# Kernel tuning notes

Hardware: AMD Instinct MI355X
Metric: run time of the kernel (lower is better)

The kernel has to match this reference:

```python
import jax, jax.numpy as jnp
import numpy as np

V, E, H, M = 32000, 512, 1024, 256
B, S = 2, 1024


def setup_inputs() -> dict:
    key = jax.random.key(0)
    ks = jax.random.split(key, 12)
    def rn(k, shape, scale=0.02):
        return jax.random.normal(k, shape, jnp.float32) * scale
    return dict(
        input_ids=jax.random.randint(ks[0], (B, S), 0, V),
        emb_W=rn(ks[1], (V, E)),
        w_ih=rn(ks[2], (3 * H, E)), w_hh=rn(ks[3], (3 * H, H)),
        b_ih=jnp.zeros((3 * H,), jnp.float32), b_hh=jnp.zeros((3 * H,), jnp.float32),
        Wq=rn(ks[4], (M, H)), bq=jnp.zeros((M,), jnp.float32),
        Wk=rn(ks[5], (M, H)), bk=jnp.zeros((M,), jnp.float32),
        Wg=rn(ks[6], (1, H)), bg=jnp.zeros((1,), jnp.float32),
        W1=rn(ks[7], (4 * E, H)), b1=jnp.zeros((4 * E,), jnp.float32),
        W2=rn(ks[8], (E, 4 * E)), b2=jnp.zeros((E,), jnp.float32),
        Wr=rn(ks[9], (E, E)), br=jnp.zeros((E,), jnp.float32),
        memory_scale=jnp.array(6.0, jnp.float32),
        output_bias=jnp.zeros((V,), jnp.float32),
    )


def _gru(emb, w_ih, w_hh, b_ih, b_hh):
    # PyTorch GRU gate order: r, z, n
    Bb = emb.shape[0]
    Hh = w_hh.shape[1]
    xp = emb @ w_ih.T + b_ih  # [B,S,3H], input projections precomputed
    def step(h, xt):
        gh = h @ w_hh.T + b_hh
        ir, iz, inn = jnp.split(xt, 3, axis=-1)
        hr, hz, hn = jnp.split(gh, 3, axis=-1)
        r = jax.nn.sigmoid(ir + hr)
        z = jax.nn.sigmoid(iz + hz)
        n = jnp.tanh(inn + r * hn)
        h = (1.0 - z) * n + z * h
        return h, h
    h0 = jnp.zeros((Bb, Hh), emb.dtype)
    _, hs = jax.lax.scan(step, h0, jnp.swapaxes(xp, 0, 1))
    return jnp.swapaxes(hs, 0, 1)  # [B,S,H]


def reference(input_ids, emb_W, w_ih, w_hh, b_ih, b_hh, Wq, bq, Wk, bk, Wg, bg,
              W1, b1, W2, b2, Wr, br, memory_scale, output_bias):
    Bb, Ss = input_ids.shape
    emb = emb_W[input_ids]                                   # [B,S,E]
    states = _gru(emb, w_ih, w_hh, b_ih, b_hh)               # [B,S,H] (dropout=0 -> identity)
    hf = jnp.square(jax.nn.relu(states @ W1.T + b1))         # [B,S,4E]
    base = hf @ W2.T + b2                                    # [B,S,E]
    residual = jax.nn.relu(base @ Wr.T + br)                 # [B,S,E]
    base_logits = base @ emb_W.T + output_bias               # [B,S,V]
    residual_logits = residual @ emb_W.T                     # [B,S,V]
    gate = jax.nn.sigmoid(states @ Wg.T + bg)                # [B,S,1]
    q = states @ Wq.T + bq                                   # [B,S,M]
    k = states @ Wk.T + bk                                   # [B,S,M]
    scores = jnp.einsum('bqd,bkd->bqk', q, k) / jnp.sqrt(jnp.float32(q.shape[-1]))
    mask = jnp.tril(jnp.ones((Ss, Ss), bool), k=-1)          # strictly-causal (diag excluded)
    scores = jnp.where(mask, scores, jnp.finfo(scores.dtype).min)
    attn = jax.nn.softmax(scores, axis=-1) * mask
    attn = attn / jnp.maximum(attn.sum(axis=-1, keepdims=True), 1e-6)
    gated = attn * (gate * memory_scale)                     # [B,S,S]
    bi = jnp.arange(Bb)[:, None, None]
    si = jnp.arange(Ss)[None, :, None]
    vi = jnp.broadcast_to(input_ids[:, None, :], (Bb, Ss, Ss))
    base_logits = base_logits.at[bi, si, vi].add(gated)      # scatter_add into vocab by token id
    return base_logits + gate * residual_logits
```

## Files before the change

### kernel.cpp

```cpp
#include <hip/hip_runtime.h>
#include <math.h>

typedef __attribute__((ext_vector_type(8))) short bf16x8;
typedef __attribute__((ext_vector_type(4))) float f32x4;

__device__ __forceinline__ unsigned short f2bf(float x) {
    unsigned u = __float_as_uint(x);
    unsigned r = (u + 0x7FFF + ((u >> 16) & 1)) >> 16;
    return (unsigned short)r;
}
__device__ __forceinline__ float bf_lo(unsigned u) { return __uint_as_float(u << 16); }
__device__ __forceinline__ float bf_hi(unsigned u) { return __uint_as_float(u & 0xffff0000u); }

#define ACT_NONE  0
#define ACT_RELU  1
#define ACT_RELU2 2

template <int ACT, bool GATHER, bool TRANSOUT>
__global__ __launch_bounds__(256) void gemm_bt(
    const float* __restrict__ A, const float* __restrict__ Bm,
    const float* __restrict__ bias, float* __restrict__ C,
    const int* __restrict__ ids, int M, int N, int K)
{
    __shared__ unsigned short as_[64][40];
    __shared__ unsigned short bs_[64][40];

    const int tid = threadIdx.x;
    const int bm = blockIdx.x, bn = blockIdx.y;
    const int r = tid >> 2, seg = tid & 3;

    const int arow = bm * 64 + r;
    const float* aptr = GATHER ? (A + (size_t)ids[arow] * K) : (A + (size_t)arow * K);
    const float* bptr = Bm + (size_t)(bn * 64 + r) * K;

    const int w = tid >> 6, lane = tid & 63;
    const int wr = w >> 1, wc = w & 1;
    const int al = lane & 15, kq = lane >> 4;

    f32x4 acc[2][2];
    for (int mi = 0; mi < 2; ++mi)
        for (int ni = 0; ni < 2; ++ni)
            acc[mi][ni] = (f32x4){0.f, 0.f, 0.f, 0.f};

    for (int k0 = 0; k0 < K; k0 += 32) {
        __syncthreads();
        {
            const float4* ap4 = (const float4*)(aptr + k0 + seg * 8);
            float4 a0 = ap4[0], a1 = ap4[1];
            uint4 pk;
            pk.x = (unsigned)f2bf(a0.x) | ((unsigned)f2bf(a0.y) << 16);
            pk.y = (unsigned)f2bf(a0.z) | ((unsigned)f2bf(a0.w) << 16);
            pk.z = (unsigned)f2bf(a1.x) | ((unsigned)f2bf(a1.y) << 16);
            pk.w = (unsigned)f2bf(a1.z) | ((unsigned)f2bf(a1.w) << 16);
            *(uint4*)&as_[r][seg * 8] = pk;

            const float4* bp4 = (const float4*)(bptr + k0 + seg * 8);
            float4 b0 = bp4[0], b1 = bp4[1];
            pk.x = (unsigned)f2bf(b0.x) | ((unsigned)f2bf(b0.y) << 16);
            pk.y = (unsigned)f2bf(b0.z) | ((unsigned)f2bf(b0.w) << 16);
            pk.z = (unsigned)f2bf(b1.x) | ((unsigned)f2bf(b1.y) << 16);
            pk.w = (unsigned)f2bf(b1.z) | ((unsigned)f2bf(b1.w) << 16);
            *(uint4*)&bs_[r][seg * 8] = pk;
        }
        __syncthreads();

        bf16x8 af[2], bfr[2];
        af[0]  = *(const bf16x8*)&as_[wr * 32 + al][kq * 8];
        af[1]  = *(const bf16x8*)&as_[wr * 32 + 16 + al][kq * 8];
        bfr[0] = *(const bf16x8*)&bs_[wc * 32 + al][kq * 8];
        bfr[1] = *(const bf16x8*)&bs_[wc * 32 + 16 + al][kq * 8];

        for (int mi = 0; mi < 2; ++mi)
            for (int ni = 0; ni < 2; ++ni)
                acc[mi][ni] = __builtin_amdgcn_mfma_f32_16x16x32_bf16(
                    af[mi], bfr[ni], acc[mi][ni], 0, 0, 0);
    }

    for (int mi = 0; mi < 2; ++mi) {
        for (int ni = 0; ni < 2; ++ni) {
            const int gcol = bn * 64 + wc * 32 + ni * 16 + al;
            const float bv = bias ? bias[gcol] : 0.f;
            for (int i = 0; i < 4; ++i) {
                const int grow = bm * 64 + wr * 32 + mi * 16 + kq * 4 + i;
                float v = acc[mi][ni][i] + bv;
                if (ACT == ACT_RELU)  v = fmaxf(v, 0.f);
                if (ACT == ACT_RELU2) { v = fmaxf(v, 0.f); v = v * v; }
                if (TRANSOUT) {
                    const int b = grow >> 10, s = grow & 1023;
                    C[((size_t)b * N + gcol) * 1024 + s] = v;
                } else {
                    C[(size_t)grow * N + gcol] = v;
                }
            }
        }
    }
}

__global__ void init_ws(float* hbuf, int* flags) {
    int t = blockIdx.x * 256 + threadIdx.x;
    if (t < 4096) hbuf[t] = 0.f;
    if (t < 128 * 32) flags[t] = 0;
}

__global__ __launch_bounds__(256, 1) void gru_kernel(
    const float* __restrict__ xp,
    const float* __restrict__ w_hh,
    const float* __restrict__ b_hh,
    float* __restrict__ states,
    float* __restrict__ hbuf,
    int* __restrict__ flags)
{
    __shared__ unsigned short wlds[24 * 1024];
    __shared__ float ghs[24][2];
    __shared__ float bh[24];

    const int wg = blockIdx.x, tid = threadIdx.x;
    const int u0 = wg * 8;

    for (int idx = tid; idx < 24 * 1024; idx += 256) {
        const int rr = idx >> 10, kk = idx & 1023;
        const int grow = (rr < 8) ? (u0 + rr) : (rr < 16) ? (1024 + u0 + rr - 8) : (2048 + u0 + rr - 16);
        wlds[idx] = f2bf(w_hh[((size_t)grow << 10) | kk]);
    }
    if (tid < 24) {
        const int rr = tid;
        const int grow = (rr < 8) ? (u0 + rr) : (rr < 16) ? (1024 + u0 + rr - 8) : (2048 + u0 + rr - 16);
        bh[rr] = b_hh[grow];
    }
    __syncthreads();

    const int w = tid >> 6, lane = tid & 63;
    const int j = tid & 7, bb = (tid >> 3) & 1;
    const float* xbase = xp + ((size_t)(bb << 10)) * 3072 + u0 + j;
    float hprev = 0.f;

    for (int t = 0; t < 1024; ++t) {
        const int p = t & 1;
        const float* src = hbuf + p * 2048;
        float* dst = hbuf + (1 - p) * 2048;

        float ir = 0.f, iz = 0.f, inn = 0.f;
        if (tid < 16) {
            const float* xr = xbase + (size_t)t * 3072;
            ir = xr[0]; iz = xr[1024]; inn = xr[2048];
        }

        if (w == 0 && t > 0) {
            const int need = t;
            for (;;) {
                int f0 = __hip_atomic_load(&flags[lane << 5],
                                           __ATOMIC_RELAXED, __HIP_MEMORY_SCOPE_AGENT);
                int f1 = __hip_atomic_load(&flags[(64 + lane) << 5],
                                           __ATOMIC_RELAXED, __HIP_MEMORY_SCOPE_AGENT);
                if (__all(f0 >= need && f1 >= need)) break;
            }
        }
        __syncthreads();

        f32x4 h_[8];
        {
            const char* pa = (const char*)src + ((size_t)lane << 5);
            const char* pb = pa + 4096;
            asm volatile(
                "global_load_dwordx4 %0, %8, off sc0 sc1\n\t"
                "global_load_dwordx4 %1, %8, off offset:16 sc0 sc1\n\t"
                "global_load_dwordx4 %2, %8, off offset:2048 sc0 sc1\n\t"
                "global_load_dwordx4 %3, %8, off offset:2064 sc0 sc1\n\t"
                "global_load_dwordx4 %4, %9, off sc0 sc1\n\t"
                "global_load_dwordx4 %5, %9, off offset:16 sc0 sc1\n\t"
                "global_load_dwordx4 %6, %9, off offset:2048 sc0 sc1\n\t"
                "global_load_dwordx4 %7, %9, off offset:2064 sc0 sc1\n\t"
                "s_waitcnt vmcnt(0)"
                : "=&v"(h_[0]), "=&v"(h_[1]), "=&v"(h_[2]), "=&v"(h_[3]),
                  "=&v"(h_[4]), "=&v"(h_[5]), "=&v"(h_[6]), "=&v"(h_[7])
                : "v"(pa), "v"(pb)
                : "memory");
        }

        float pacc[6][2];
        #pragma unroll
        for (int rr6 = 0; rr6 < 6; ++rr6) {
            pacc[rr6][0] = 0.f; pacc[rr6][1] = 0.f;
            const uint4* wr4 = (const uint4*)&wlds[(w * 6 + rr6) << 10];
            #pragma unroll
            for (int c = 0; c < 2; ++c) {
                const uint4 wv = wr4[c * 64 + lane];
                const float w0 = bf_lo(wv.x), w1 = bf_hi(wv.x);
                const float w2 = bf_lo(wv.y), w3 = bf_hi(wv.y);
                const float w4 = bf_lo(wv.z), w5 = bf_hi(wv.z);
                const float w6 = bf_lo(wv.w), w7 = bf_hi(wv.w);
                {
                    const f32x4 ha = h_[c * 2], hb2 = h_[c * 2 + 1];
                    pacc[rr6][0] += w0 * ha.x + w1 * ha.y + w2 * ha.z + w3 * ha.w
                                  + w4 * hb2.x + w5 * hb2.y + w6 * hb2.z + w7 * hb2.w;
                }
                {
                    const f32x4 ha = h_[4 + c * 2], hb2 = h_[4 + c * 2 + 1];
                    pacc[rr6][1] += w0 * ha.x + w1 * ha.y + w2 * ha.z + w3 * ha.w
                                  + w4 * hb2.x + w5 * hb2.y + w6 * hb2.z + w7 * hb2.w;
                }
            }
        }
        #pragma unroll
        for (int off = 32; off > 0; off >>= 1) {
            #pragma unroll
            for (int rr6 = 0; rr6 < 6; ++rr6) {
                pacc[rr6][0] += __shfl_xor(pacc[rr6][0], off);
                pacc[rr6][1] += __shfl_xor(pacc[rr6][1], off);
            }
        }
        if (lane == 0) {
            #pragma unroll
            for (int rr6 = 0; rr6 < 6; ++rr6) {
                ghs[w * 6 + rr6][0] = pacc[rr6][0];
                ghs[w * 6 + rr6][1] = pacc[rr6][1];
            }
        }
        __syncthreads();

        if (tid < 16) {
            const float hr  = ghs[j][bb]      + bh[j];
            const float hz  = ghs[8 + j][bb]  + bh[8 + j];
            const float hnv = ghs[16 + j][bb] + bh[16 + j];
            const float rg = 1.f / (1.f + __expf(-(ir + hr)));
            const float zg = 1.f / (1.f + __expf(-(iz + hz)));
            const float ng = tanhf(inn + rg * hnv);
            const float hnew = (1.f - zg) * ng + zg * hprev;
            hprev = hnew;
            const int row = (bb << 10) | t;
            states[(size_t)row * 1024 + u0 + j] = hnew;
            __hip_atomic_store(&dst[(bb << 10) + u0 + j], hnew,
                               __ATOMIC_RELAXED, __HIP_MEMORY_SCOPE_AGENT);
        }
        if (w == 0) {
            asm volatile("s_waitcnt vmcnt(0)" ::: "memory");
            if (lane == 0)
                __hip_atomic_store(&flags[wg << 5], t + 1,
                                   __ATOMIC_RELAXED, __HIP_MEMORY_SCOPE_AGENT);
        }
    }
}

__global__ __launch_bounds__(256) void gate_kernel(
    const float* __restrict__ states, const float* __restrict__ Wg,
    const float* __restrict__ bg, float* __restrict__ gate)
{
    const int w = threadIdx.x >> 6, lane = threadIdx.x & 63;
    const int row = blockIdx.x * 4 + w;
    const float4* sr = (const float4*)(states + (size_t)row * 1024);
    const float4* wr = (const float4*)Wg;
    float p = 0.f;
    for (int c = 0; c < 4; ++c) {
        const float4 sv = sr[c * 64 + lane];
        const float4 wv = wr[c * 64 + lane];
        p += sv.x * wv.x + sv.y * wv.y + sv.z * wv.z + sv.w * wv.w;
    }
    for (int off = 32; off > 0; off >>= 1) p += __shfl_xor(p, off);
    if (lane == 0) gate[row] = 1.f / (1.f + __expf(-(p + bg[0])));
}

__global__ __launch_bounds__(256) void combined_kernel(
    const float* __restrict__ base, const float* __restrict__ resid,
    const float* __restrict__ gate, float* __restrict__ comb)
{
    const int idx = blockIdx.x * 256 + threadIdx.x;
    const int row = idx >> 9;
    comb[idx] = base[idx] + gate[row] * resid[idx];
}

__global__ __launch_bounds__(256) void attn_scatter(
    const float* __restrict__ q,
    const float* __restrict__ kT,
    const float* __restrict__ gate,
    const float* __restrict__ mscale,
    const int* __restrict__ ids,
    float* __restrict__ out)
{
    const int i = blockIdx.x, b = blockIdx.y, t = threadIdx.x;
    if (i == 0) return;
    __shared__ float qs[256];
    __shared__ float red[256];

    qs[t] = q[((size_t)((b << 10) | i)) * 256 + t];
    __syncthreads();

    const int j0 = t * 4;
    float s[4] = {0.f, 0.f, 0.f, 0.f};
    const float* kb = kT + (size_t)b * 256 * 1024;
    if (j0 < i) {
        for (int kk = 0; kk < 256; ++kk) {
            const float qv = qs[kk];
            const float4 kv = *(const float4*)(kb + (size_t)kk * 1024 + j0);
            s[0] += qv * kv.x; s[1] += qv * kv.y; s[2] += qv * kv.z; s[3] += qv * kv.w;
        }
    }
    const float scale = 0.0625f;
    float mx = -1e30f;
    for (int e = 0; e < 4; ++e)
        if (j0 + e < i) { s[e] *= scale; mx = fmaxf(mx, s[e]); }

    red[t] = mx; __syncthreads();
    for (int o = 128; o > 0; o >>= 1) {
        if (t < o) red[t] = fmaxf(red[t], red[t + o]);
        __syncthreads();
    }
    const float m = red[0];
    __syncthreads();

    float p[4]; float ssum = 0.f;
    for (int e = 0; e < 4; ++e) {
        if (j0 + e < i) { p[e] = __expf(s[e] - m); ssum += p[e]; }
        else p[e] = 0.f;
    }
    red[t] = ssum; __syncthreads();
    for (int o = 128; o > 0; o >>= 1) {
        if (t < o) red[t] += red[t + o];
        __syncthreads();
    }
    const float denom = fmaxf(red[0], 1e-6f);
    const float g6 = gate[(b << 10) | i] * mscale[0] / denom;

    float* orow = out + ((size_t)((b << 10) | i)) * 32000;
    const int* idr = ids + (b << 10);
    for (int e = 0; e < 4; ++e)
        if (j0 + e < i) atomicAdd(&orow[idr[j0 + e]], p[e] * g6);
}

extern "C" void kernel_launch(void* const* d_in, const int* in_sizes, int n_in,
                              void* d_out, int out_size, void* d_ws, size_t ws_size,
                              hipStream_t stream)
{
    const int*   ids     = (const int*)  d_in[0];
    const float* emb_W   = (const float*)d_in[1];
    const float* w_ih    = (const float*)d_in[2];
    const float* w_hh    = (const float*)d_in[3];
    const float* b_ih    = (const float*)d_in[4];
    const float* b_hh    = (const float*)d_in[5];
    const float* Wq      = (const float*)d_in[6];
    const float* bq      = (const float*)d_in[7];
    const float* Wk      = (const float*)d_in[8];
    const float* bk      = (const float*)d_in[9];
    const float* Wg      = (const float*)d_in[10];
    const float* bg      = (const float*)d_in[11];
    const float* W1      = (const float*)d_in[12];
    const float* b1      = (const float*)d_in[13];
    const float* W2      = (const float*)d_in[14];
    const float* b2      = (const float*)d_in[15];
    const float* Wr      = (const float*)d_in[16];
    const float* br      = (const float*)d_in[17];
    const float* mscale  = (const float*)d_in[18];
    const float* out_b   = (const float*)d_in[19];
    float* out = (float*)d_out;

    float* ws = (float*)d_ws;
    float* xp     = ws;
    float* states = xp     + (size_t)2048 * 3072;
    float* hf     = states + (size_t)2048 * 1024;
    float* base   = hf     + (size_t)2048 * 2048;
    float* resid  = base   + (size_t)2048 * 512;
    float* qv     = resid  + (size_t)2048 * 512;
    float* kT     = qv     + (size_t)2048 * 256;
    float* comb   = kT     + (size_t)2 * 256 * 1024;
    float* gate   = comb   + (size_t)2048 * 512;
    float* hbuf   = gate   + 2048;
    int*   flags  = (int*)(hbuf + 4096);

    dim3 blk(256);

    gemm_bt<ACT_NONE, true, false><<<dim3(32, 48), blk, 0, stream>>>(
        emb_W, w_ih, b_ih, xp, ids, 2048, 3072, 512);

    init_ws<<<16, blk, 0, stream>>>(hbuf, flags);
    gru_kernel<<<128, blk, 0, stream>>>(xp, w_hh, b_hh, states, hbuf, flags);

    gemm_bt<ACT_RELU2, false, false><<<dim3(32, 32), blk, 0, stream>>>(
        states, W1, b1, hf, nullptr, 2048, 2048, 1024);

    gemm_bt<ACT_NONE, false, false><<<dim3(32, 8), blk, 0, stream>>>(
        hf, W2, b2, base, nullptr, 2048, 512, 2048);

    gemm_bt<ACT_RELU, false, false><<<dim3(32, 8), blk, 0, stream>>>(
        base, Wr, br, resid, nullptr, 2048, 512, 512);

    gate_kernel<<<512, blk, 0, stream>>>(states, Wg, bg, gate);

    gemm_bt<ACT_NONE, false, false><<<dim3(32, 4), blk, 0, stream>>>(
        states, Wq, bq, qv, nullptr, 2048, 256, 1024);
    gemm_bt<ACT_NONE, false, true><<<dim3(32, 4), blk, 0, stream>>>(
        states, Wk, bk, kT, nullptr, 2048, 256, 1024);

    combined_kernel<<<4096, blk, 0, stream>>>(base, resid, gate, comb);

    gemm_bt<ACT_NONE, false, false><<<dim3(32, 500), blk, 0, stream>>>(
        comb, emb_W, out_b, out, nullptr, 2048, 32000, 512);

    attn_scatter<<<dim3(1024, 2), blk, 0, stream>>>(qv, kT, gate, mscale, ids, out);
}
```

Before: 4.237 ms.

## Fuse GRU step flags into hidden-state values as tagged pairs

Replaces the separate per-workgroup flag array and spin-then-load sequence in the persistent GRU kernel with (value, step tag) pairs written in one 8-byte store. Each wave now polls the hidden-state buffer directly until every tag matches the current step, which removes one global round trip and a block-wide barrier per timestep from the serial recurrence. It doubles the bytes read per poll, all four waves spin independently, and the ghs scratch is double-buffered because the barrier is gone.

```diff
diff --git a/kernel.cpp b/kernel.cpp
--- a/kernel.cpp
+++ b/kernel.cpp
@@ -96,10 +96,9 @@
     }
 }
 
-__global__ void init_ws(float* hbuf, int* flags) {
+__global__ void init_ws(float* hbuf2) {
     int t = blockIdx.x * 256 + threadIdx.x;
-    if (t < 4096) hbuf[t] = 0.f;
-    if (t < 128 * 32) flags[t] = 0;
+    if (t < 8192) hbuf2[t] = 0.f;
 }
 
 __global__ __launch_bounds__(256, 1) void gru_kernel(
@@ -107,11 +106,10 @@
     const float* __restrict__ w_hh,
     const float* __restrict__ b_hh,
     float* __restrict__ states,
-    float* __restrict__ hbuf,
-    int* __restrict__ flags)
+    float* __restrict__ hbuf2)
 {
     __shared__ unsigned short wlds[24 * 1024];
-    __shared__ float ghs[24][2];
+    __shared__ float ghs[2][24][2];
     __shared__ float bh[24];
 
     const int wg = blockIdx.x, tid = threadIdx.x;
@@ -136,8 +134,8 @@
 
     for (int t = 0; t < 1024; ++t) {
         const int p = t & 1;
-        const float* src = hbuf + p * 2048;
-        float* dst = hbuf + (1 - p) * 2048;
+        const float* src = hbuf2 + p * 4096;
+        float* dst = hbuf2 + (1 - p) * 4096;
 
         float ir = 0.f, iz = 0.f, inn = 0.f;
         if (tid < 16) {
@@ -145,36 +143,45 @@
             ir = xr[0]; iz = xr[1024]; inn = xr[2048];
         }
 
-        if (w == 0 && t > 0) {
-            const int need = t;
+        f32x4 q[16];
+        {
+            const char* b0 = (const char*)src + (lane << 6);
+            const char* b1 = b0 + 4096;
+            const char* b2 = b0 + 8192;
+            const char* b3 = b0 + 12288;
+            const int expect = t;
             for (;;) {
-                int f0 = __hip_atomic_load(&flags[lane << 5],
-                                           __ATOMIC_RELAXED, __HIP_MEMORY_SCOPE_AGENT);
-                int f1 = __hip_atomic_load(&flags[(64 + lane) << 5],
-                                           __ATOMIC_RELAXED, __HIP_MEMORY_SCOPE_AGENT);
-                if (__all(f0 >= need && f1 >= need)) break;
+                asm volatile(
+                    "global_load_dwordx4 %0, %16, off sc0 sc1\n\t"
+                    "global_load_dwordx4 %1, %16, off offset:16 sc0 sc1\n\t"
+                    "global_load_dwordx4 %2, %16, off offset:32 sc0 sc1\n\t"
+                    "global_load_dwordx4 %3, %16, off offset:48 sc0 sc1\n\t"
+                    "global_load_dwordx4 %4, %17, off sc0 sc1\n\t"
+                    "global_load_dwordx4 %5, %17, off offset:16 sc0 sc1\n\t"
+                    "global_load_dwordx4 %6, %17, off offset:32 sc0 sc1\n\t"
+                    "global_load_dwordx4 %7, %17, off offset:48 sc0 sc1\n\t"
+                    "global_load_dwordx4 %8, %18, off sc0 sc1\n\t"
+                    "global_load_dwordx4 %9, %18, off offset:16 sc0 sc1\n\t"
+                    "global_load_dwordx4 %10, %18, off offset:32 sc0 sc1\n\t"
+                    "global_load_dwordx4 %11, %18, off offset:48 sc0 sc1\n\t"
+                    "global_load_dwordx4 %12, %19, off sc0 sc1\n\t"
+                    "global_load_dwordx4 %13, %19, off offset:16 sc0 sc1\n\t"
+                    "global_load_dwordx4 %14, %19, off offset:32 sc0 sc1\n\t"
+                    "global_load_dwordx4 %15, %19, off offset:48 sc0 sc1\n\t"
+                    "s_waitcnt vmcnt(0)"
+                    : "=&v"(q[0]), "=&v"(q[1]), "=&v"(q[2]), "=&v"(q[3]),
+                      "=&v"(q[4]), "=&v"(q[5]), "=&v"(q[6]), "=&v"(q[7]),
+                      "=&v"(q[8]), "=&v"(q[9]), "=&v"(q[10]), "=&v"(q[11]),
+                      "=&v"(q[12]), "=&v"(q[13]), "=&v"(q[14]), "=&v"(q[15])
+                    : "v"(b0), "v"(b1), "v"(b2), "v"(b3)
+                    : "memory");
+                bool ok = true;
+                #pragma unroll
+                for (int k = 0; k < 16; ++k)
+                    ok = ok && (__float_as_int(q[k].y) == expect)
+                            && (__float_as_int(q[k].w) == expect);
+                if (__all(ok)) break;
             }
-        }
-        __syncthreads();
-
-        f32x4 h_[8];
-        {
-            const char* pa = (const char*)src + ((size_t)lane << 5);
-            const char* pb = pa + 4096;
-            asm volatile(
-                "global_load_dwordx4 %0, %8, off sc0 sc1\n\t"
-                "global_load_dwordx4 %1, %8, off offset:16 sc0 sc1\n\t"
-                "global_load_dwordx4 %2, %8, off offset:2048 sc0 sc1\n\t"
-                "global_load_dwordx4 %3, %8, off offset:2064 sc0 sc1\n\t"
-                "global_load_dwordx4 %4, %9, off sc0 sc1\n\t"
-                "global_load_dwordx4 %5, %9, off offset:16 sc0 sc1\n\t"
-                "global_load_dwordx4 %6, %9, off offset:2048 sc0 sc1\n\t"
-                "global_load_dwordx4 %7, %9, off offset:2064 sc0 sc1\n\t"
-                "s_waitcnt vmcnt(0)"
-                : "=&v"(h_[0]), "=&v"(h_[1]), "=&v"(h_[2]), "=&v"(h_[3]),
-                  "=&v"(h_[4]), "=&v"(h_[5]), "=&v"(h_[6]), "=&v"(h_[7])
-                : "v"(pa), "v"(pb)
-                : "memory");
         }
 
         float pacc[6][2];
@@ -189,16 +196,15 @@
                 const float w2 = bf_lo(wv.y), w3 = bf_hi(wv.y);
                 const float w4 = bf_lo(wv.z), w5 = bf_hi(wv.z);
                 const float w6 = bf_lo(wv.w), w7 = bf_hi(wv.w);
-                {
-                    const f32x4 ha = h_[c * 2], hb2 = h_[c * 2 + 1];
-                    pacc[rr6][0] += w0 * ha.x + w1 * ha.y + w2 * ha.z + w3 * ha.w
-                                  + w4 * hb2.x + w5 * hb2.y + w6 * hb2.z + w7 * hb2.w;
-                }
-                {
-                    const f32x4 ha = h_[4 + c * 2], hb2 = h_[4 + c * 2 + 1];
-                    pacc[rr6][1] += w0 * ha.x + w1 * ha.y + w2 * ha.z + w3 * ha.w
-                                  + w4 * hb2.x + w5 * hb2.y + w6 * hb2.z + w7 * hb2.w;
-                }
+                const int c4 = c * 4;
+                pacc[rr6][0] += w0 * q[c4].x     + w1 * q[c4].z
+                              + w2 * q[c4 + 1].x + w3 * q[c4 + 1].z
+                              + w4 * q[c4 + 2].x + w5 * q[c4 + 2].z
+                              + w6 * q[c4 + 3].x + w7 * q[c4 + 3].z;
+                pacc[rr6][1] += w0 * q[8 + c4].x     + w1 * q[8 + c4].z
+                              + w2 * q[8 + c4 + 1].x + w3 * q[8 + c4 + 1].z
+                              + w4 * q[8 + c4 + 2].x + w5 * q[8 + c4 + 2].z
+                              + w6 * q[8 + c4 + 3].x + w7 * q[8 + c4 + 3].z;
             }
         }
         #pragma unroll
@@ -212,16 +218,16 @@
         if (lane == 0) {
             #pragma unroll
             for (int rr6 = 0; rr6 < 6; ++rr6) {
-                ghs[w * 6 + rr6][0] = pacc[rr6][0];
-                ghs[w * 6 + rr6][1] = pacc[rr6][1];
+                ghs[p][w * 6 + rr6][0] = pacc[rr6][0];
+                ghs[p][w * 6 + rr6][1] = pacc[rr6][1];
             }
         }
         __syncthreads();
 
         if (tid < 16) {
-            const float hr  = ghs[j][bb]      + bh[j];
-            const float hz  = ghs[8 + j][bb]  + bh[8 + j];
-            const float hnv = ghs[16 + j][bb] + bh[16 + j];
+            const float hr  = ghs[p][j][bb]      + bh[j];
+            const float hz  = ghs[p][8 + j][bb]  + bh[8 + j];
+            const float hnv = ghs[p][16 + j][bb] + bh[16 + j];
             const float rg = 1.f / (1.f + __expf(-(ir + hr)));
             const float zg = 1.f / (1.f + __expf(-(iz + hz)));
             const float ng = tanhf(inn + rg * hnv);
@@ -229,14 +235,12 @@
             hprev = hnew;
             const int row = (bb << 10) | t;
             states[(size_t)row * 1024 + u0 + j] = hnew;
-            __hip_atomic_store(&dst[(bb << 10) + u0 + j], hnew,
-                               __ATOMIC_RELAXED, __HIP_MEMORY_SCOPE_AGENT);
-        }
-        if (w == 0) {
-            asm volatile("s_waitcnt vmcnt(0)" ::: "memory");
-            if (lane == 0)
-                __hip_atomic_store(&flags[wg << 5], t + 1,
-                                   __ATOMIC_RELAXED, __HIP_MEMORY_SCOPE_AGENT);
+            uint2 pk;
+            pk.x = __float_as_uint(hnew);
+            pk.y = (unsigned)(t + 1);
+            float* daddr = dst + 2 * ((bb << 10) + u0 + j);
+            asm volatile("global_store_dwordx2 %0, %1, off sc0 sc1"
+                         :: "v"(daddr), "v"(pk) : "memory");
         }
     }
 }
@@ -362,16 +366,15 @@
     float* kT     = qv     + (size_t)2048 * 256;
     float* comb   = kT     + (size_t)2 * 256 * 1024;
     float* gate   = comb   + (size_t)2048 * 512;
-    float* hbuf   = gate   + 2048;
-    int*   flags  = (int*)(hbuf + 4096);
+    float* hbuf2  = gate   + 2048;
 
     dim3 blk(256);
 
     gemm_bt<ACT_NONE, true, false><<<dim3(32, 48), blk, 0, stream>>>(
         emb_W, w_ih, b_ih, xp, ids, 2048, 3072, 512);
 
-    init_ws<<<16, blk, 0, stream>>>(hbuf, flags);
-    gru_kernel<<<128, blk, 0, stream>>>(xp, w_hh, b_hh, states, hbuf, flags);
+    init_ws<<<32, blk, 0, stream>>>(hbuf2);
+    gru_kernel<<<128, blk, 0, stream>>>(xp, w_hh, b_hh, states, hbuf2);
 
     gemm_bt<ACT_RELU2, false, false><<<dim3(32, 32), blk, 0, stream>>>(
         states, W1, b1, hf, nullptr, 2048, 2048, 1024);
```

Measured after the change: 7.662 ms. +80.8%, slower.

## Make each GRU wave compute its own units and drop per-step block barriers

Applied to the files above, without the earlier changes.

Each wave now owns two hidden units for both batch rows, with each half-wave handling one batch row. It computes the gate dot products, reduces them with shuffles within 32 lanes, and applies the GRU update locally. This removes both __syncthreads and the LDS staging of gate sums. Flags become packed per-wave counters (512 ints, read as two dwordx4 loads per lane), and every wave polls them itself. The weight layout in LDS is reshuffled to match the new lane mapping. The trade-offs are more polling traffic, since all four waves spin, and per-wave flag publishing.

```diff
diff --git a/kernel.cpp b/kernel.cpp
--- a/kernel.cpp
+++ b/kernel.cpp
@@ -3,6 +3,7 @@
 
 typedef __attribute__((ext_vector_type(8))) short bf16x8;
 typedef __attribute__((ext_vector_type(4))) float f32x4;
+typedef __attribute__((ext_vector_type(4))) int i32x4;
 
 __device__ __forceinline__ unsigned short f2bf(float x) {
     unsigned u = __float_as_uint(x);
@@ -99,7 +100,7 @@
 __global__ void init_ws(float* hbuf, int* flags) {
     int t = blockIdx.x * 256 + threadIdx.x;
     if (t < 4096) hbuf[t] = 0.f;
-    if (t < 128 * 32) flags[t] = 0;
+    if (t < 512) flags[t] = 0;
 }
 
 __global__ __launch_bounds__(256, 1) void gru_kernel(
@@ -111,132 +112,132 @@
     int* __restrict__ flags)
 {
     __shared__ unsigned short wlds[24 * 1024];
-    __shared__ float ghs[24][2];
-    __shared__ float bh[24];
 
     const int wg = blockIdx.x, tid = threadIdx.x;
     const int u0 = wg * 8;
+    const int w = tid >> 6, lane = tid & 63;
+    const int half = lane >> 5, hl = lane & 31;
 
     for (int idx = tid; idx < 24 * 1024; idx += 256) {
         const int rr = idx >> 10, kk = idx & 1023;
-        const int grow = (rr < 8) ? (u0 + rr) : (rr < 16) ? (1024 + u0 + rr - 8) : (2048 + u0 + rr - 16);
-        wlds[idx] = f2bf(w_hh[((size_t)grow << 10) | kk]);
-    }
-    if (tid < 24) {
-        const int rr = tid;
-        const int grow = (rr < 8) ? (u0 + rr) : (rr < 16) ? (1024 + u0 + rr - 8) : (2048 + u0 + rr - 16);
-        bh[rr] = b_hh[grow];
-    }
+        const int w_ = rr / 6, q = rr - 6 * w_;
+        const int g = q >> 1, u = q & 1;
+        const int grow = (g << 10) + u0 + 2 * w_ + u;
+        const int hl_ = kk >> 5, rem = kk & 31, c_ = rem >> 3, e = rem & 7;
+        wlds[(rr << 10) + c_ * 256 + hl_ * 8 + e] =
+            f2bf(w_hh[((size_t)grow << 10) | kk]);
+    }
+
+    const int uA = u0 + 2 * w;
+    const float2 bhr = *(const float2*)&b_hh[uA];
+    const float2 bhz = *(const float2*)&b_hh[1024 + uA];
+    const float2 bhn = *(const float2*)&b_hh[2048 + uA];
+
     __syncthreads();
 
-    const int w = tid >> 6, lane = tid & 63;
-    const int j = tid & 7, bb = (tid >> 3) & 1;
-    const float* xbase = xp + ((size_t)(bb << 10)) * 3072 + u0 + j;
-    float hprev = 0.f;
+    float hpA = 0.f, hpB = 0.f;
 
     for (int t = 0; t < 1024; ++t) {
         const int p = t & 1;
         const float* src = hbuf + p * 2048;
         float* dst = hbuf + (1 - p) * 2048;
 
-        float ir = 0.f, iz = 0.f, inn = 0.f;
-        if (tid < 16) {
-            const float* xr = xbase + (size_t)t * 3072;
-            ir = xr[0]; iz = xr[1024]; inn = xr[2048];
-        }
-
-        if (w == 0 && t > 0) {
+        float2 xr_ = make_float2(0.f, 0.f);
+        float2 xz_ = make_float2(0.f, 0.f);
+        float2 xn_ = make_float2(0.f, 0.f);
+        if (hl == 0) {
+            const float* xr = xp + (size_t)((half << 10) | t) * 3072 + uA;
+            xr_ = *(const float2*)xr;
+            xz_ = *(const float2*)(xr + 1024);
+            xn_ = *(const float2*)(xr + 2048);
+        }
+
+        if (t > 0) {
+            const char* fa = (const char*)flags + (lane << 5);
             const int need = t;
+            i32x4 f0, f1;
             for (;;) {
-                int f0 = __hip_atomic_load(&flags[lane << 5],
-                                           __ATOMIC_RELAXED, __HIP_MEMORY_SCOPE_AGENT);
-                int f1 = __hip_atomic_load(&flags[(64 + lane) << 5],
-                                           __ATOMIC_RELAXED, __HIP_MEMORY_SCOPE_AGENT);
-                if (__all(f0 >= need && f1 >= need)) break;
+                asm volatile(
+                    "global_load_dwordx4 %0, %2, off sc0 sc1\n\t"
+                    "global_load_dwordx4 %1, %2, off offset:16 sc0 sc1\n\t"
+                    "s_waitcnt vmcnt(0)"
+                    : "=&v"(f0), "=&v"(f1) : "v"(fa) : "memory");
+                int m = f0.x < f0.y ? f0.x : f0.y;
+                m = m < f0.z ? m : f0.z;  m = m < f0.w ? m : f0.w;
+                m = m < f1.x ? m : f1.x;  m = m < f1.y ? m : f1.y;
+                m = m < f1.z ? m : f1.z;  m = m < f1.w ? m : f1.w;
+                if (__all(m >= need)) break;
             }
         }
-        __syncthreads();
 
         f32x4 h_[8];
         {
-            const char* pa = (const char*)src + ((size_t)lane << 5);
-            const char* pb = pa + 4096;
+            const char* hb = (const char*)src + (half << 12) + (hl << 7);
             asm volatile(
                 "global_load_dwordx4 %0, %8, off sc0 sc1\n\t"
                 "global_load_dwordx4 %1, %8, off offset:16 sc0 sc1\n\t"
-                "global_load_dwordx4 %2, %8, off offset:2048 sc0 sc1\n\t"
-                "global_load_dwordx4 %3, %8, off offset:2064 sc0 sc1\n\t"
-                "global_load_dwordx4 %4, %9, off sc0 sc1\n\t"
-                "global_load_dwordx4 %5, %9, off offset:16 sc0 sc1\n\t"
-                "global_load_dwordx4 %6, %9, off offset:2048 sc0 sc1\n\t"
-                "global_load_dwordx4 %7, %9, off offset:2064 sc0 sc1\n\t"
+                "global_load_dwordx4 %2, %8, off offset:32 sc0 sc1\n\t"
+                "global_load_dwordx4 %3, %8, off offset:48 sc0 sc1\n\t"
+                "global_load_dwordx4 %4, %8, off offset:64 sc0 sc1\n\t"
+                "global_load_dwordx4 %5, %8, off offset:80 sc0 sc1\n\t"
+                "global_load_dwordx4 %6, %8, off offset:96 sc0 sc1\n\t"
+                "global_load_dwordx4 %7, %8, off offset:112 sc0 sc1\n\t"
                 "s_waitcnt vmcnt(0)"
                 : "=&v"(h_[0]), "=&v"(h_[1]), "=&v"(h_[2]), "=&v"(h_[3]),
                   "=&v"(h_[4]), "=&v"(h_[5]), "=&v"(h_[6]), "=&v"(h_[7])
-                : "v"(pa), "v"(pb)
+                : "v"(hb)
                 : "memory");
         }
 
-        float pacc[6][2];
+        float pacc[6];
         #pragma unroll
-        for (int rr6 = 0; rr6 < 6; ++rr6) {
-            pacc[rr6][0] = 0.f; pacc[rr6][1] = 0.f;
-            const uint4* wr4 = (const uint4*)&wlds[(w * 6 + rr6) << 10];
+        for (int q = 0; q < 6; ++q) {
+            const uint4* wr4 = (const uint4*)&wlds[(w * 6 + q) << 10];
+            float a = 0.f;
             #pragma unroll
-            for (int c = 0; c < 2; ++c) {
-                const uint4 wv = wr4[c * 64 + lane];
-                const float w0 = bf_lo(wv.x), w1 = bf_hi(wv.x);
-                const float w2 = bf_lo(wv.y), w3 = bf_hi(wv.y);
-                const float w4 = bf_lo(wv.z), w5 = bf_hi(wv.z);
-                const float w6 = bf_lo(wv.w), w7 = bf_hi(wv.w);
-                {
-                    const f32x4 ha = h_[c * 2], hb2 = h_[c * 2 + 1];
-                    pacc[rr6][0] += w0 * ha.x + w1 * ha.y + w2 * ha.z + w3 * ha.w
-                                  + w4 * hb2.x + w5 * hb2.y + w6 * hb2.z + w7 * hb2.w;
-                }
-                {
-                    const f32x4 ha = h_[4 + c * 2], hb2 = h_[4 + c * 2 + 1];
-                    pacc[rr6][1] += w0 * ha.x + w1 * ha.y + w2 * ha.z + w3 * ha.w
-                                  + w4 * hb2.x + w5 * hb2.y + w6 * hb2.z + w7 * hb2.w;
-                }
+            for (int c = 0; c < 4; ++c) {
+                const uint4 wv = wr4[c * 32 + hl];
+                const f32x4 ha = h_[c * 2], hb2 = h_[c * 2 + 1];
+                a += bf_lo(wv.x) * ha.x  + bf_hi(wv.x) * ha.y
+                   + bf_lo(wv.y) * ha.z  + bf_hi(wv.y) * ha.w
+                   + bf_lo(wv.z) * hb2.x + bf_hi(wv.z) * hb2.y
+                   + bf_lo(wv.w) * hb2.z + bf_hi(wv.w) * hb2.w;
             }
+            pacc[q] = a;
         }
         #pragma unroll
-        for (int off = 32; off > 0; off >>= 1) {
+        for (int off = 16; off > 0; off >>= 1) {
             #pragma unroll
-            for (int rr6 = 0; rr6 < 6; ++rr6) {
-                pacc[rr6][0] += __shfl_xor(pacc[rr6][0], off);
-                pacc[rr6][1] += __shfl_xor(pacc[rr6][1], off);
-            }
-        }
+            for (int q = 0; q < 6; ++q)
+                pacc[q] += __shfl_xor(pacc[q], off);
+        }
+
+        if (hl == 0) {
+            const float rA = 1.f / (1.f + __expf(-(xr_.x + pacc[0] + bhr.x)));
+            const float zA = 1.f / (1.f + __expf(-(xz_.x + pacc[2] + bhz.x)));
+            const float nA = tanhf(xn_.x + rA * (pacc[4] + bhn.x));
+            const float hA = (1.f - zA) * nA + zA * hpA;
+            hpA = hA;
+            const float rB = 1.f / (1.f + __expf(-(xr_.y + pacc[1] + bhr.y)));
+            const float zB = 1.f / (1.f + __expf(-(xz_.y + pacc[3] + bhz.y)));
+            const float nB = tanhf(xn_.y + rB * (pacc[5] + bhn.y));
+            const float hB = (1.f - zB) * nB + zB * hpB;
+            hpB = hB;
+
+            *(float2*)&states[(size_t)((half << 10) | t) * 1024 + uA] =
+                make_float2(hA, hB);
+
+            float2 hv = make_float2(hA, hB);
+            float* daddr = dst + (half << 10) + uA;
+            asm volatile("global_store_dwordx2 %0, %1, off sc0 sc1"
+                         :: "v"(daddr), "v"(hv) : "memory");
+        }
+        asm volatile("s_waitcnt vmcnt(0)" ::: "memory");
         if (lane == 0) {
-            #pragma unroll
-            for (int rr6 = 0; rr6 < 6; ++rr6) {
-                ghs[w * 6 + rr6][0] = pacc[rr6][0];
-                ghs[w * 6 + rr6][1] = pacc[rr6][1];
-            }
-        }
-        __syncthreads();
-
-        if (tid < 16) {
-            const float hr  = ghs[j][bb]      + bh[j];
-            const float hz  = ghs[8 + j][bb]  + bh[8 + j];
-            const float hnv = ghs[16 + j][bb] + bh[16 + j];
-            const float rg = 1.f / (1.f + __expf(-(ir + hr)));
-            const float zg = 1.f / (1.f + __expf(-(iz + hz)));
-            const float ng = tanhf(inn + rg * hnv);
-            const float hnew = (1.f - zg) * ng + zg * hprev;
-            hprev = hnew;
-            const int row = (bb << 10) | t;
-            states[(size_t)row * 1024 + u0 + j] = hnew;
-            __hip_atomic_store(&dst[(bb << 10) + u0 + j], hnew,
-                               __ATOMIC_RELAXED, __HIP_MEMORY_SCOPE_AGENT);
-        }
-        if (w == 0) {
-            asm volatile("s_waitcnt vmcnt(0)" ::: "memory");
-            if (lane == 0)
-                __hip_atomic_store(&flags[wg << 5], t + 1,
-                                   __ATOMIC_RELAXED, __HIP_MEMORY_SCOPE_AGENT);
+            int* faddr = flags + (wg << 2) + w;
+            const int tv = t + 1;
+            asm volatile("global_store_dword %0, %1, off sc0 sc1"
+                         :: "v"(faddr), "v"(tv) : "memory");
         }
     }
 }
```

Result: slower. 7.998 ms (+88.8%).
